# Performance work log

Measured on AMD Instinct MI355X. Metric: run time of the kernel, lower is better.

Reference implementation:

```python
import jax, jax.numpy as jnp
import numpy as np

B, LQ, LA = 128, 128, 512
VOCAB, EMB, FILT, K = 50000, 300, 400, 3
EPS = 1e-8


def setup_inputs() -> dict:
    key = jax.random.key(0)
    kq, ka, ke, kw, kb, kW = jax.random.split(key, 6)
    questions = jax.random.randint(kq, (B, LQ), 0, VOCAB + 1, dtype=jnp.int32)
    answers = jax.random.randint(ka, (B, LA), 0, VOCAB + 1, dtype=jnp.int32)
    emb = jax.random.normal(ke, (VOCAB + 1, EMB), dtype=jnp.float32) * 0.1
    emb = emb.at[0].set(0.0)  # padding_idx=0
    fan_in = EMB * K
    bound = 1.0 / np.sqrt(fan_in)
    conv_w = jax.random.uniform(kw, (FILT, EMB, K), jnp.float32, -bound, bound)
    conv_b = jax.random.uniform(kb, (FILT,), jnp.float32, -bound, bound)
    W = jax.random.normal(kW, (FILT, FILT), dtype=jnp.float32)  # init.normal_(std=1)
    return {"questions": questions, "answers": answers, "emb": emb,
            "conv_w": conv_w, "conv_b": conv_b, "W": W}


def _encode(tokens, emb, conv_w, conv_b):
    # tokens [B,L] -> embed [B,L,E] -> transpose to NCH [B,E,L] -> conv1d pad=1
    x = emb[tokens].transpose(0, 2, 1)
    y = jax.lax.conv_general_dilated(
        x, conv_w, window_strides=(1,), padding=[(1, 1)],
        dimension_numbers=("NCH", "OIH", "NCH"))
    return y + conv_b[None, :, None]  # [B, FILT, L]


def reference(questions, answers, emb, conv_w, conv_b, W):
    Q = _encode(questions, emb, conv_w, conv_b)  # [B,F,Lq]
    A = _encode(answers, emb, conv_w, conv_b)    # [B,F,La]
    # G = tanh(Q^T W A)  -> [B, Lq, La]
    G = jnp.tanh(jnp.einsum("bfq,fg,bga->bqa", Q, W, A))
    roQ = jax.nn.softmax(jnp.max(G, axis=2), axis=1)  # [B,Lq]
    roA = jax.nn.softmax(jnp.max(G, axis=1), axis=1)  # [B,La]
    rQ = jnp.einsum("bfq,bq->bf", Q, roQ)  # [B,F]
    rA = jnp.einsum("bfa,ba->bf", A, roA)  # [B,F]
    nQ = jnp.maximum(jnp.linalg.norm(rQ, axis=1), EPS)
    nA = jnp.maximum(jnp.linalg.norm(rA, axis=1), EPS)
    return jnp.sum(rQ * rA, axis=1) / (nQ * nA)  # [B]
```

## Files before the change

kernel.cpp:

```cpp
#include <hip/hip_runtime.h>
#include <hip/hip_bf16.h>

#define BB   128
#define LQ   128
#define LA   512
#define EMBD 300
#define FILT 400
#define KW   3

#define NT   25
#define KC   30
#define KCF  13
#define MT   64

typedef unsigned short u16;
typedef unsigned int   u32;
typedef __attribute__((ext_vector_type(4))) int    i32x4;
typedef __attribute__((ext_vector_type(4))) float  f32x4;
typedef __attribute__((ext_vector_type(8))) __bf16 bf16x8;

__device__ __forceinline__ u16 f2b(float f){
  u32 u = __float_as_uint(f);
  u32 r = (u + 0x7FFFu + ((u >> 16) & 1u)) >> 16;
  return (u16)r;
}
__device__ __forceinline__ u32 encf(float f){
  u32 u = __float_as_uint(f);
  return (u & 0x80000000u) ? ~u : (u | 0x80000000u);
}
__device__ __forceinline__ float decf(u32 k){
  u32 u = (k & 0x80000000u) ? (k ^ 0x80000000u) : ~k;
  return __uint_as_float(u);
}
__device__ __forceinline__ bf16x8 bzero(){
  i32x4 z; z.x = 0; z.y = 0; z.z = 0; z.w = 0;
  return __builtin_bit_cast(bf16x8, z);
}

__global__ void k_prep(const float* __restrict__ cw, const float* __restrict__ W,
                       u32* __restrict__ wTf, u32* __restrict__ wF){
  int idx = blockIdx.x * 256 + threadIdx.x;
  const int N1 = KC * NT * 64;
  const int N2 = KCF * NT * 64;
  if (idx < N1){
    int kc  = idx / (NT * 64);
    int rem = idx - kc * (NT * 64);
    int nt  = rem >> 6;
    int lane = rem & 63;
    int n = nt * 16 + (lane & 15);
    int quad = lane >> 4;
    u32 pack[4];
    #pragma unroll
    for (int d = 0; d < 4; d++){
      u16 h[2];
      #pragma unroll
      for (int s = 0; s < 2; s++){
        int kp = kc * 32 + quad * 8 + 2 * d + s;
        int kk = kp / 320, e = kp - kk * 320;
        float v = (e < EMBD) ? cw[(size_t)n * (EMBD * KW) + e * KW + kk] : 0.f;
        h[s] = f2b(v);
      }
      pack[d] = (u32)h[0] | ((u32)h[1] << 16);
    }
    i32x4 o; o.x = pack[0]; o.y = pack[1]; o.z = pack[2]; o.w = pack[3];
    *((i32x4*)wTf + idx) = o;
  } else if (idx < N1 + N2){
    int id2 = idx - N1;
    int kc  = id2 / (NT * 64);
    int rem = id2 - kc * (NT * 64);
    int nt  = rem >> 6;
    int lane = rem & 63;
    int n = nt * 16 + (lane & 15);
    int quad = lane >> 4;
    u32 pack[4];
    #pragma unroll
    for (int d = 0; d < 4; d++){
      u16 h[2];
      #pragma unroll
      for (int s = 0; s < 2; s++){
        int k = kc * 32 + quad * 8 + 2 * d + s;
        float v = (k < FILT) ? W[(size_t)k * FILT + n] : 0.f;
        h[s] = f2b(v);
      }
      pack[d] = (u32)h[0] | ((u32)h[1] << 16);
    }
    i32x4 o; o.x = pack[0]; o.y = pack[1]; o.z = pack[2]; o.w = pack[3];
    *((i32x4*)wF + id2) = o;
  }
}

__global__ __launch_bounds__(512, 4) void k_encode_all(const int* __restrict__ qtok,
    const int* __restrict__ atok, const float* __restrict__ emb,
    const u32* __restrict__ wTf, const float* __restrict__ bias,
    u16* __restrict__ outQ, u16* __restrict__ outA){
  __shared__ u16 At[66 * 328];

  const int tid  = threadIdx.x;
  const int w    = tid >> 6;
  const int lane = tid & 63;
  const int col  = lane & 15;
  const int quad = lane >> 4;
  const bool has4 = (w == 0);
  const int nA = BB * LA / MT;
  const bool isA = ((int)blockIdx.x < nA);
  const int bi = isA ? blockIdx.x : (blockIdx.x - nA);
  const int L  = isA ? LA : LQ;
  const int* toks = isA ? atok : qtok;
  u16* out = isA ? outA : outQ;
  const int row0 = bi * MT;
  const int b    = row0 / L;
  const int l0   = row0 - b * L;

  int tk[10], cc[10], rws[10];
  #pragma unroll
  for (int u = 0; u < 10; u++){
    int idx = tid + 512 * u;
    tk[u] = -1; cc[u] = 0; rws[u] = 0;
    if (idx < 66 * 75){
      int r = idx / 75, c4 = idx - r * 75;
      int pos = l0 - 1 + r;
      cc[u] = c4;
      rws[u] = (r * 328 + c4 * 4) >> 1;
      if ((unsigned)pos < (unsigned)L) tk[u] = toks[b * L + pos];
    }
  }
  for (int i = tid; i < 66 * 328 / 2; i += 512) ((u32*)At)[i] = 0u;
  __syncthreads();
  {
    const float4* emb4 = (const float4*)emb;
    #pragma unroll
    for (int g = 0; g < 2; g++){
      float4 v[5];
      #pragma unroll
      for (int u = 0; u < 5; u++){
        int uu = g * 5 + u;
        if (tk[uu] >= 0) v[u] = emb4[(size_t)tk[uu] * 75 + cc[uu]];
      }
      #pragma unroll
      for (int u = 0; u < 5; u++){
        int uu = g * 5 + u;
        if (tk[uu] >= 0){
          u32 p0 = (u32)f2b(v[u].x) | ((u32)f2b(v[u].y) << 16);
          u32 p1 = (u32)f2b(v[u].z) | ((u32)f2b(v[u].w) << 16);
          ((u32*)At)[rws[uu]]     = p0;
          ((u32*)At)[rws[uu] + 1] = p1;
        }
      }
    }
  }

  f32x4 acc[4][4];
  #pragma unroll
  for (int j = 0; j < 4; j++)
    #pragma unroll
    for (int mf = 0; mf < 4; mf++)
      acc[j][mf] = (f32x4){0.f, 0.f, 0.f, 0.f};

  __syncthreads();

  const i32x4* wTfp = (const i32x4*)wTf;
  i32x4 Bb[2][4];
  {
    #pragma unroll
    for (int j = 0; j < 3; j++) Bb[0][j] = wTfp[(size_t)(w + 8 * j) * 64 + lane];
    if (has4) Bb[0][3] = wTfp[(size_t)24 * 64 + lane];
  }
  #pragma unroll
  for (int kc = 0; kc < KC; kc++){
    const int cur = kc & 1;
    if (kc + 1 < KC){
      const i32x4* s = wTfp + (size_t)(kc + 1) * (NT * 64) + lane;
      #pragma unroll
      for (int j = 0; j < 3; j++) Bb[cur ^ 1][j] = s[(w + 8 * j) * 64];
      if (has4) Bb[cur ^ 1][3] = s[24 * 64];
    }
    const int kk = kc / 10, e0 = (kc - kk * 10) * 32;
    const int ebase = e0 + quad * 8;
    bf16x8 a[4];
    #pragma unroll
    for (int mf = 0; mf < 4; mf++)
      a[mf] = __builtin_bit_cast(bf16x8, *(const i32x4*)(At + (mf * 16 + col + kk) * 328 + ebase));
    #pragma unroll
    for (int j = 0; j < 3; j++){
      bf16x8 bf = __builtin_bit_cast(bf16x8, Bb[cur][j]);
      #pragma unroll
      for (int mf = 0; mf < 4; mf++)
        acc[j][mf] = __builtin_amdgcn_mfma_f32_16x16x32_bf16(a[mf], bf, acc[j][mf], 0, 0, 0);
    }
    if (has4){
      bf16x8 bf = __builtin_bit_cast(bf16x8, Bb[cur][3]);
      #pragma unroll
      for (int mf = 0; mf < 4; mf++)
        acc[3][mf] = __builtin_amdgcn_mfma_f32_16x16x32_bf16(a[mf], bf, acc[3][mf], 0, 0, 0);
    }
  }

  #pragma unroll
  for (int j = 0; j < 4; j++){
    if (j == 3 && !has4) continue;
    int n = ((j < 3) ? (w + 8 * j) : 24) * 16 + col;
    float bv = bias[n];
    #pragma unroll
    for (int mf = 0; mf < 4; mf++){
      int rbase = row0 + mf * 16 + quad * 4;
      #pragma unroll
      for (int r = 0; r < 4; r++)
        out[(size_t)(rbase + r) * FILT + n] = f2b(acc[j][mf][r] + bv);
    }
  }
}

__global__ __launch_bounds__(512) void k_mid(const u16* __restrict__ QT,
    const u32* __restrict__ wF, const u16* __restrict__ AT,
    u32* __restrict__ rme, u32* __restrict__ cme){
  __shared__ u16 Ts[64 * 408];
  __shared__ float cpart[512][5];
  const int tid  = threadIdx.x;
  const int w    = tid >> 6;
  const int lane = tid & 63;
  const int col  = lane & 15;
  const int quad = lane >> 4;
  const int qh   = blockIdx.x;
  const int b    = blockIdx.y;
  const int wq   = w & 3;
  const int wh   = w >> 2;

  {
    const int bnt = wh ? 13 : 0;
    const int cnt = wh ? 12 : 13;
    const u16* arow = QT + (size_t)(b * LQ + qh * 64 + wq * 16 + col) * FILT;
    const i32x4* wFp = (const i32x4*)wF;
    for (int ntc = 0; ntc < 3; ntc++){
      const int nleft = cnt - ntc * 5;
      f32x4 acc[5];
      #pragma unroll
      for (int j = 0; j < 5; j++) acc[j] = (f32x4){0.f, 0.f, 0.f, 0.f};
      i32x4 Ab[2], Bb[2][5];
      Ab[0] = *(const i32x4*)(arow + quad * 8);
      #pragma unroll
      for (int j = 0; j < 5; j++)
        if (j < nleft) Bb[0][j] = wFp[(size_t)(bnt + ntc * 5 + j) * 64 + lane];
      for (int kc = 0; kc < KCF; kc++){
        const int cur = kc & 1;
        if (kc + 1 < KCF){
          Ab[cur ^ 1] = *(const i32x4*)(arow + (kc + 1) * 32 + quad * 8);
          #pragma unroll
          for (int j = 0; j < 5; j++)
            if (j < nleft)
              Bb[cur ^ 1][j] = wFp[((size_t)(kc + 1) * NT + bnt + ntc * 5 + j) * 64 + lane];
        }
        bf16x8 a = __builtin_bit_cast(bf16x8, Ab[cur]);
        #pragma unroll
        for (int j = 0; j < 5; j++)
          if (j < nleft)
            acc[j] = __builtin_amdgcn_mfma_f32_16x16x32_bf16(a,
                       __builtin_bit_cast(bf16x8, Bb[cur][j]), acc[j], 0, 0, 0);
      }
      #pragma unroll
      for (int j = 0; j < 5; j++){
        if (j < nleft){
          int g = (bnt + ntc * 5 + j) * 16 + col;
          #pragma unroll
          for (int r = 0; r < 4; r++)
            Ts[(wq * 16 + quad * 4 + r) * 408 + g] = f2b(acc[j][r]);
        }
      }
    }
  }
  __syncthreads();

  float rm[4];
  #pragma unroll
  for (int r = 0; r < 4; r++) rm[r] = -3.4e38f;
  const u16* Tsrow = Ts + (wq * 16 + col) * 408;
  for (int atg = 0; atg < 2; atg++){
    f32x4 acc[8];
    #pragma unroll
    for (int i = 0; i < 8; i++) acc[i] = (f32x4){0.f, 0.f, 0.f, 0.f};
    const u16* ar = AT + (size_t)(b * LA + wh * 256 + atg * 128 + col) * FILT;
    i32x4 Ab2[2], Bb2[2][8];
    Ab2[0] = *(const i32x4*)(Tsrow + quad * 8);
    #pragma unroll
    for (int i = 0; i < 8; i++)
      Bb2[0][i] = *(const i32x4*)(ar + (size_t)(i * 16) * FILT + quad * 8);
    for (int kc = 0; kc < KCF; kc++){
      const int cur = kc & 1;
      if (kc + 1 < KCF){
        int off = (kc + 1) * 32 + quad * 8;
        Ab2[cur ^ 1] = *(const i32x4*)(Tsrow + off);
        #pragma unroll
        for (int i = 0; i < 8; i++)
          Bb2[cur ^ 1][i] = *(const i32x4*)(ar + (size_t)(i * 16) * FILT + off);
      }
      const bool live = (kc < 12) || (quad < 2);
      bf16x8 a = live ? __builtin_bit_cast(bf16x8, Ab2[cur]) : bzero();
      #pragma unroll
      for (int i = 0; i < 8; i++)
        acc[i] = __builtin_amdgcn_mfma_f32_16x16x32_bf16(a,
                   __builtin_bit_cast(bf16x8, Bb2[cur][i]), acc[i], 0, 0, 0);
    }
    #pragma unroll
    for (int i = 0; i < 8; i++){
      float cmx = fmaxf(fmaxf(acc[i][0], acc[i][1]), fmaxf(acc[i][2], acc[i][3]));
      cmx = fmaxf(cmx, __shfl_xor(cmx, 16));
      cmx = fmaxf(cmx, __shfl_xor(cmx, 32));
      if (quad == 0) cpart[wh * 256 + atg * 128 + i * 16 + col][wq] = cmx;
      #pragma unroll
      for (int r = 0; r < 4; r++) rm[r] = fmaxf(rm[r], acc[i][r]);
    }
  }
  #pragma unroll
  for (int r = 0; r < 4; r++){
    float m = rm[r];
    m = fmaxf(m, __shfl_xor(m, 1));
    m = fmaxf(m, __shfl_xor(m, 2));
    m = fmaxf(m, __shfl_xor(m, 4));
    m = fmaxf(m, __shfl_xor(m, 8));
    if (col == 0)
      atomicMax(&rme[b * LQ + qh * 64 + wq * 16 + quad * 4 + r], encf(m));
  }
  __syncthreads();
  {
    float m = cpart[tid][0];
    #pragma unroll
    for (int s = 1; s < 4; s++) m = fmaxf(m, cpart[tid][s]);
    atomicMax(&cme[b * LA + tid], encf(m));
  }
}

__global__ __launch_bounds__(256) void k_pool(const u16* __restrict__ QT,
    const u16* __restrict__ AT, const u32* __restrict__ rme,
    const u32* __restrict__ cme, float* __restrict__ rqp, float* __restrict__ rap){
  __shared__ float sq[128];
  __shared__ float sa[512];
  __shared__ float red[4];
  const int s = blockIdx.x, b = blockIdx.y, tid = threadIdx.x;
  if (tid < 128) sq[tid] = tanhf(decf(rme[b * LQ + tid]));
  sa[tid]       = tanhf(decf(cme[b * LA + tid]));
  sa[tid + 256] = tanhf(decf(cme[b * LA + 256 + tid]));
  __syncthreads();
  if (tid < 64){
    float m = fmaxf(sq[tid], sq[tid + 64]);
    #pragma unroll
    for (int off = 32; off; off >>= 1) m = fmaxf(m, __shfl_down(m, off));
    if (tid == 0) red[0] = m;
  } else if (tid < 128){
    int l = tid - 64;
    float m = sa[l];
    #pragma unroll
    for (int i = 1; i < 8; i++) m = fmaxf(m, sa[l + 64 * i]);
    #pragma unroll
    for (int off = 32; off; off >>= 1) m = fmaxf(m, __shfl_down(m, off));
    if (l == 0) red[1] = m;
  }
  __syncthreads();
  if (tid < 128) sq[tid] = __expf(sq[tid] - red[0]);
  sa[tid]       = __expf(sa[tid] - red[1]);
  sa[tid + 256] = __expf(sa[tid + 256] - red[1]);
  __syncthreads();
  if (tid < 64){
    float v = sq[tid] + sq[tid + 64];
    #pragma unroll
    for (int off = 32; off; off >>= 1) v += __shfl_down(v, off);
    if (tid == 0) red[2] = v;
  } else if (tid < 128){
    int l = tid - 64;
    float v = 0.f;
    #pragma unroll
    for (int i = 0; i < 8; i++) v += sa[l + 64 * i];
    #pragma unroll
    for (int off = 32; off; off >>= 1) v += __shfl_down(v, off);
    if (l == 0) red[3] = v;
  }
  __syncthreads();
  if (tid < 128) sq[tid] *= (1.f / red[2]);
  sa[tid]       *= (1.f / red[3]);
  sa[tid + 256] *= (1.f / red[3]);
  __syncthreads();
  if (tid < FILT / 2){
    const u32* qp = (const u32*)(QT + (size_t)(b * LQ + s * 32) * FILT) + tid;
    const u32* ap = (const u32*)(AT + (size_t)(b * LA + s * 128) * FILT) + tid;
    float rq0 = 0.f, rq1 = 0.f, ra0 = 0.f, ra1 = 0.f;
    for (int q = 0; q < 32; q++){
      u32 u = qp[q * (FILT / 2)];
      float wv = sq[s * 32 + q];
      rq0 += __uint_as_float(u << 16) * wv;
      rq1 += __uint_as_float(u & 0xFFFF0000u) * wv;
    }
    for (int a = 0; a < 128; a++){
      u32 u = ap[a * (FILT / 2)];
      float wv = sa[s * 128 + a];
      ra0 += __uint_as_float(u << 16) * wv;
      ra1 += __uint_as_float(u & 0xFFFF0000u) * wv;
    }
    size_t base = ((size_t)b * 4 + s) * FILT + 2 * tid;
    rqp[base] = rq0; rqp[base + 1] = rq1;
    rap[base] = ra0; rap[base + 1] = ra1;
  }
}

__global__ __launch_bounds__(256) void k_cos(const float* __restrict__ rqp,
    const float* __restrict__ rap, float* __restrict__ outp){
  __shared__ float rd[4], r1[4], r2[4];
  int b = blockIdx.x, tid = threadIdx.x;
  int lane = tid & 63, w = tid >> 6;
  float d = 0.f, n1 = 0.f, n2 = 0.f;
  for (int f = tid; f < FILT; f += 256){
    size_t base = (size_t)b * 4 * FILT + f;
    float rq = rqp[base] + rqp[base + FILT] + rqp[base + 2 * FILT] + rqp[base + 3 * FILT];
    float ra = rap[base] + rap[base + FILT] + rap[base + 2 * FILT] + rap[base + 3 * FILT];
    d += rq * ra; n1 += rq * rq; n2 += ra * ra;
  }
  #pragma unroll
  for (int off = 32; off; off >>= 1){
    d  += __shfl_down(d, off);
    n1 += __shfl_down(n1, off);
    n2 += __shfl_down(n2, off);
  }
  if (lane == 0){ rd[w] = d; r1[w] = n1; r2[w] = n2; }
  __syncthreads();
  if (tid == 0){
    float D  = rd[0] + rd[1] + rd[2] + rd[3];
    float N1 = r1[0] + r1[1] + r1[2] + r1[3];
    float N2 = r2[0] + r2[1] + r2[2] + r2[3];
    outp[b] = D / (fmaxf(sqrtf(N1), 1e-8f) * fmaxf(sqrtf(N2), 1e-8f));
  }
}

extern "C" void kernel_launch(void* const* d_in, const int* in_sizes, int n_in,
                              void* d_out, int out_size, void* d_ws, size_t ws_size,
                              hipStream_t stream){
  const int*   qtok = (const int*)d_in[0];
  const int*   atok = (const int*)d_in[1];
  const float* emb  = (const float*)d_in[2];
  const float* cw   = (const float*)d_in[3];
  const float* cb   = (const float*)d_in[4];
  const float* W    = (const float*)d_in[5];
  float* outp = (float*)d_out;

  char* ws = (char*)d_ws;
  size_t off = 0;
  auto alloc = [&](size_t bytes) -> char* {
    char* p = ws + off;
    off = (off + bytes + 255) & ~(size_t)255;
    return p;
  };
  u32*   wTf = (u32*)alloc((size_t)KC * NT * 64 * 16);
  u32*   wF  = (u32*)alloc((size_t)KCF * NT * 64 * 16);
  u16*   QT  = (u16*)alloc((size_t)BB * LQ * FILT * 2);
  u16*   AT  = (u16*)alloc((size_t)BB * LA * FILT * 2);
  u32*   rme = (u32*)alloc((size_t)BB * LQ * 4);
  u32*   cme = (u32*)alloc((size_t)BB * LA * 4);
  float* rqp = (float*)alloc((size_t)BB * 4 * FILT * 4);
  float* rap = (float*)alloc((size_t)BB * 4 * FILT * 4);

  hipMemsetAsync(rme, 0, (size_t)BB * LQ * 4 + (size_t)BB * LA * 4, stream);

  const int NPREP = KC * NT * 64 + KCF * NT * 64;
  const int nA = BB * LA / MT;
  const int nQ = BB * LQ / MT;
  k_prep<<<dim3((NPREP + 255) / 256), 256, 0, stream>>>(cw, W, wTf, wF);
  k_encode_all<<<dim3(nA + nQ), 512, 0, stream>>>(qtok, atok, emb, wTf, cb, QT, AT);
  k_mid<<<dim3(2, BB), 512, 0, stream>>>(QT, wF, AT, rme, cme);
  k_pool<<<dim3(4, BB), 256, 0, stream>>>(QT, AT, rme, cme, rqp, rap);
  k_cos<<<dim3(BB), 256, 0, stream>>>(rqp, rap, outp);
}
```

Measured before the change: 234.6 us.

## Split k_mid into 32-row query tiles, widen pool split, fold memset into prep

k_mid now handles 32 query rows per block instead of 64, doubling the grid to 4x128 blocks. The first GEMM is reorganised so each wave owns a set of N tiles across both 16-row fragments, and the second GEMM uses half the A tiles per wave. LDS use drops and launch bounds now request two blocks per CU. k_pool is split into 8 slices with the partial buffers and k_cos widened to match, and the rme/cme zeroing moves from hipMemsetAsync into k_prep. The intent is more parallelism and occupancy and one fewer launch, at the cost of reloading the W fragments per block and more atomics.

```diff
diff --git a/kernel.cpp b/kernel.cpp
--- a/kernel.cpp
+++ b/kernel.cpp
@@ -38,10 +38,12 @@
 }
 
 __global__ void k_prep(const float* __restrict__ cw, const float* __restrict__ W,
-                       u32* __restrict__ wTf, u32* __restrict__ wF){
+                       u32* __restrict__ wTf, u32* __restrict__ wF,
+                       u32* __restrict__ rmecme){
   int idx = blockIdx.x * 256 + threadIdx.x;
   const int N1 = KC * NT * 64;
   const int N2 = KCF * NT * 64;
+  const int N3 = BB * (LQ + LA);
   if (idx < N1){
     int kc  = idx / (NT * 64);
     int rem = idx - kc * (NT * 64);
@@ -86,6 +88,8 @@
     }
     i32x4 o; o.x = pack[0]; o.y = pack[1]; o.z = pack[2]; o.w = pack[3];
     *((i32x4*)wF + id2) = o;
+  } else if (idx < N1 + N2 + N3){
+    rmecme[idx - N1 - N2] = 0u;
   }
 }
 
@@ -210,78 +214,91 @@
   }
 }
 
-__global__ __launch_bounds__(512) void k_mid(const u16* __restrict__ QT,
+__global__ __launch_bounds__(512, 2) void k_mid(const u16* __restrict__ QT,
     const u32* __restrict__ wF, const u16* __restrict__ AT,
     u32* __restrict__ rme, u32* __restrict__ cme){
-  __shared__ u16 Ts[64 * 408];
-  __shared__ float cpart[512][5];
+  __shared__ u16 Ts[32 * 408];
+  __shared__ float cpart[512][3];
   const int tid  = threadIdx.x;
   const int w    = tid >> 6;
   const int lane = tid & 63;
   const int col  = lane & 15;
   const int quad = lane >> 4;
-  const int qh   = blockIdx.x;
+  const int qq   = blockIdx.x;
   const int b    = blockIdx.y;
-  const int wq   = w & 3;
-  const int wh   = w >> 2;
 
   {
-    const int bnt = wh ? 13 : 0;
-    const int cnt = wh ? 12 : 13;
-    const u16* arow = QT + (size_t)(b * LQ + qh * 64 + wq * 16 + col) * FILT;
+    const bool has4 = (w == 0);
+    const u16* arow0 = QT + (size_t)(b * LQ + qq * 32 + col) * FILT;
+    const u16* arow1 = QT + (size_t)(b * LQ + qq * 32 + 16 + col) * FILT;
     const i32x4* wFp = (const i32x4*)wF;
-    for (int ntc = 0; ntc < 3; ntc++){
-      const int nleft = cnt - ntc * 5;
-      f32x4 acc[5];
-      #pragma unroll
-      for (int j = 0; j < 5; j++) acc[j] = (f32x4){0.f, 0.f, 0.f, 0.f};
-      i32x4 Ab[2], Bb[2][5];
-      Ab[0] = *(const i32x4*)(arow + quad * 8);
-      #pragma unroll
-      for (int j = 0; j < 5; j++)
-        if (j < nleft) Bb[0][j] = wFp[(size_t)(bnt + ntc * 5 + j) * 64 + lane];
-      for (int kc = 0; kc < KCF; kc++){
-        const int cur = kc & 1;
-        if (kc + 1 < KCF){
-          Ab[cur ^ 1] = *(const i32x4*)(arow + (kc + 1) * 32 + quad * 8);
-          #pragma unroll
-          for (int j = 0; j < 5; j++)
-            if (j < nleft)
-              Bb[cur ^ 1][j] = wFp[((size_t)(kc + 1) * NT + bnt + ntc * 5 + j) * 64 + lane];
-        }
-        bf16x8 a = __builtin_bit_cast(bf16x8, Ab[cur]);
+    f32x4 acc1[4][2];
+    #pragma unroll
+    for (int j = 0; j < 4; j++)
+      #pragma unroll
+      for (int mf = 0; mf < 2; mf++)
+        acc1[j][mf] = (f32x4){0.f, 0.f, 0.f, 0.f};
+    i32x4 Ab[2][2], Bb[2][4];
+    {
+      Ab[0][0] = *(const i32x4*)(arow0 + quad * 8);
+      Ab[0][1] = *(const i32x4*)(arow1 + quad * 8);
+      #pragma unroll
+      for (int j = 0; j < 3; j++) Bb[0][j] = wFp[(size_t)(w + 8 * j) * 64 + lane];
+      if (has4) Bb[0][3] = wFp[(size_t)24 * 64 + lane];
+    }
+    for (int kc = 0; kc < KCF; kc++){
+      const int cur = kc & 1;
+      if (kc + 1 < KCF){
+        int off = (kc + 1) * 32 + quad * 8;
+        Ab[cur ^ 1][0] = *(const i32x4*)(arow0 + off);
+        Ab[cur ^ 1][1] = *(const i32x4*)(arow1 + off);
+        const i32x4* s = wFp + (size_t)(kc + 1) * (NT * 64) + lane;
         #pragma unroll
-        for (int j = 0; j < 5; j++)
-          if (j < nleft)
-            acc[j] = __builtin_amdgcn_mfma_f32_16x16x32_bf16(a,
-                       __builtin_bit_cast(bf16x8, Bb[cur][j]), acc[j], 0, 0, 0);
-      }
-      #pragma unroll
-      for (int j = 0; j < 5; j++){
-        if (j < nleft){
-          int g = (bnt + ntc * 5 + j) * 16 + col;
-          #pragma unroll
-          for (int r = 0; r < 4; r++)
-            Ts[(wq * 16 + quad * 4 + r) * 408 + g] = f2b(acc[j][r]);
-        }
-      }
-    }
-  }
-  __syncthreads();
-
+        for (int j = 0; j < 3; j++) Bb[cur ^ 1][j] = s[(w + 8 * j) * 64];
+        if (has4) Bb[cur ^ 1][3] = s[24 * 64];
+      }
+      bf16x8 a0 = __builtin_bit_cast(bf16x8, Ab[cur][0]);
+      bf16x8 a1 = __builtin_bit_cast(bf16x8, Ab[cur][1]);
+      #pragma unroll
+      for (int j = 0; j < 3; j++){
+        bf16x8 bf = __builtin_bit_cast(bf16x8, Bb[cur][j]);
+        acc1[j][0] = __builtin_amdgcn_mfma_f32_16x16x32_bf16(a0, bf, acc1[j][0], 0, 0, 0);
+        acc1[j][1] = __builtin_amdgcn_mfma_f32_16x16x32_bf16(a1, bf, acc1[j][1], 0, 0, 0);
+      }
+      if (has4){
+        bf16x8 bf = __builtin_bit_cast(bf16x8, Bb[cur][3]);
+        acc1[3][0] = __builtin_amdgcn_mfma_f32_16x16x32_bf16(a0, bf, acc1[3][0], 0, 0, 0);
+        acc1[3][1] = __builtin_amdgcn_mfma_f32_16x16x32_bf16(a1, bf, acc1[3][1], 0, 0, 0);
+      }
+    }
+    #pragma unroll
+    for (int j = 0; j < 4; j++){
+      if (j == 3 && !has4) continue;
+      int g = ((j < 3) ? (w + 8 * j) : 24) * 16 + col;
+      #pragma unroll
+      for (int mf = 0; mf < 2; mf++)
+        #pragma unroll
+        for (int r = 0; r < 4; r++)
+          Ts[(mf * 16 + quad * 4 + r) * 408 + g] = f2b(acc1[j][mf][r]);
+    }
+  }
+  __syncthreads();
+
+  const int qt2 = w & 1;
+  const int aq  = w >> 1;
   float rm[4];
   #pragma unroll
   for (int r = 0; r < 4; r++) rm[r] = -3.4e38f;
-  const u16* Tsrow = Ts + (wq * 16 + col) * 408;
+  const u16* Tsrow = Ts + (qt2 * 16 + col) * 408;
   for (int atg = 0; atg < 2; atg++){
-    f32x4 acc[8];
-    #pragma unroll
-    for (int i = 0; i < 8; i++) acc[i] = (f32x4){0.f, 0.f, 0.f, 0.f};
-    const u16* ar = AT + (size_t)(b * LA + wh * 256 + atg * 128 + col) * FILT;
-    i32x4 Ab2[2], Bb2[2][8];
+    f32x4 acc[4];
+    #pragma unroll
+    for (int i = 0; i < 4; i++) acc[i] = (f32x4){0.f, 0.f, 0.f, 0.f};
+    const u16* ar = AT + (size_t)(b * LA + aq * 128 + atg * 64 + col) * FILT;
+    i32x4 Ab2[2], Bb2[2][4];
     Ab2[0] = *(const i32x4*)(Tsrow + quad * 8);
     #pragma unroll
-    for (int i = 0; i < 8; i++)
+    for (int i = 0; i < 4; i++)
       Bb2[0][i] = *(const i32x4*)(ar + (size_t)(i * 16) * FILT + quad * 8);
     for (int kc = 0; kc < KCF; kc++){
       const int cur = kc & 1;
@@ -289,22 +306,22 @@
         int off = (kc + 1) * 32 + quad * 8;
         Ab2[cur ^ 1] = *(const i32x4*)(Tsrow + off);
         #pragma unroll
-        for (int i = 0; i < 8; i++)
+        for (int i = 0; i < 4; i++)
           Bb2[cur ^ 1][i] = *(const i32x4*)(ar + (size_t)(i * 16) * FILT + off);
       }
       const bool live = (kc < 12) || (quad < 2);
       bf16x8 a = live ? __builtin_bit_cast(bf16x8, Ab2[cur]) : bzero();
       #pragma unroll
-      for (int i = 0; i < 8; i++)
+      for (int i = 0; i < 4; i++)
         acc[i] = __builtin_amdgcn_mfma_f32_16x16x32_bf16(a,
                    __builtin_bit_cast(bf16x8, Bb2[cur][i]), acc[i], 0, 0, 0);
     }
     #pragma unroll
-    for (int i = 0; i < 8; i++){
+    for (int i = 0; i < 4; i++){
       float cmx = fmaxf(fmaxf(acc[i][0], acc[i][1]), fmaxf(acc[i][2], acc[i][3]));
       cmx = fmaxf(cmx, __shfl_xor(cmx, 16));
       cmx = fmaxf(cmx, __shfl_xor(cmx, 32));
-      if (quad == 0) cpart[wh * 256 + atg * 128 + i * 16 + col][wq] = cmx;
+      if (quad == 0) cpart[aq * 128 + atg * 64 + i * 16 + col][qt2] = cmx;
       #pragma unroll
       for (int r = 0; r < 4; r++) rm[r] = fmaxf(rm[r], acc[i][r]);
     }
@@ -317,13 +334,11 @@
     m = fmaxf(m, __shfl_xor(m, 4));
     m = fmaxf(m, __shfl_xor(m, 8));
     if (col == 0)
-      atomicMax(&rme[b * LQ + qh * 64 + wq * 16 + quad * 4 + r], encf(m));
+      atomicMax(&rme[b * LQ + qq * 32 + qt2 * 16 + quad * 4 + r], encf(m));
   }
   __syncthreads();
   {
-    float m = cpart[tid][0];
-    #pragma unroll
-    for (int s = 1; s < 4; s++) m = fmaxf(m, cpart[tid][s]);
+    float m = fmaxf(cpart[tid][0], cpart[tid][1]);
     atomicMax(&cme[b * LA + tid], encf(m));
   }
 }
@@ -378,22 +393,22 @@
   sa[tid + 256] *= (1.f / red[3]);
   __syncthreads();
   if (tid < FILT / 2){
-    const u32* qp = (const u32*)(QT + (size_t)(b * LQ + s * 32) * FILT) + tid;
-    const u32* ap = (const u32*)(AT + (size_t)(b * LA + s * 128) * FILT) + tid;
+    const u32* qp = (const u32*)(QT + (size_t)(b * LQ + s * 16) * FILT) + tid;
+    const u32* ap = (const u32*)(AT + (size_t)(b * LA + s * 64) * FILT) + tid;
     float rq0 = 0.f, rq1 = 0.f, ra0 = 0.f, ra1 = 0.f;
-    for (int q = 0; q < 32; q++){
+    for (int q = 0; q < 16; q++){
       u32 u = qp[q * (FILT / 2)];
-      float wv = sq[s * 32 + q];
+      float wv = sq[s * 16 + q];
       rq0 += __uint_as_float(u << 16) * wv;
       rq1 += __uint_as_float(u & 0xFFFF0000u) * wv;
     }
-    for (int a = 0; a < 128; a++){
+    for (int a = 0; a < 64; a++){
       u32 u = ap[a * (FILT / 2)];
-      float wv = sa[s * 128 + a];
+      float wv = sa[s * 64 + a];
       ra0 += __uint_as_float(u << 16) * wv;
       ra1 += __uint_as_float(u & 0xFFFF0000u) * wv;
     }
-    size_t base = ((size_t)b * 4 + s) * FILT + 2 * tid;
+    size_t base = ((size_t)b * 8 + s) * FILT + 2 * tid;
     rqp[base] = rq0; rqp[base + 1] = rq1;
     rap[base] = ra0; rap[base + 1] = ra1;
   }
@@ -406,9 +421,13 @@
   int lane = tid & 63, w = tid >> 6;
   float d = 0.f, n1 = 0.f, n2 = 0.f;
   for (int f = tid; f < FILT; f += 256){
-    size_t base = (size_t)b * 4 * FILT + f;
-    float rq = rqp[base] + rqp[base + FILT] + rqp[base + 2 * FILT] + rqp[base + 3 * FILT];
-    float ra = rap[base] + rap[base + FILT] + rap[base + 2 * FILT] + rap[base + 3 * FILT];
+    size_t base = (size_t)b * 8 * FILT + f;
+    float rq = 0.f, ra = 0.f;
+    #pragma unroll
+    for (int s = 0; s < 8; s++){
+      rq += rqp[base + s * FILT];
+      ra += rap[base + s * FILT];
+    }
     d += rq * ra; n1 += rq * rq; n2 += ra * ra;
   }
   #pragma unroll
@@ -451,17 +470,15 @@
   u16*   AT  = (u16*)alloc((size_t)BB * LA * FILT * 2);
   u32*   rme = (u32*)alloc((size_t)BB * LQ * 4);
   u32*   cme = (u32*)alloc((size_t)BB * LA * 4);
-  float* rqp = (float*)alloc((size_t)BB * 4 * FILT * 4);
-  float* rap = (float*)alloc((size_t)BB * 4 * FILT * 4);
-
-  hipMemsetAsync(rme, 0, (size_t)BB * LQ * 4 + (size_t)BB * LA * 4, stream);
-
-  const int NPREP = KC * NT * 64 + KCF * NT * 64;
+  float* rqp = (float*)alloc((size_t)BB * 8 * FILT * 4);
+  float* rap = (float*)alloc((size_t)BB * 8 * FILT * 4);
+
+  const int NPREP = KC * NT * 64 + KCF * NT * 64 + BB * (LQ + LA);
   const int nA = BB * LA / MT;
   const int nQ = BB * LQ / MT;
-  k_prep<<<dim3((NPREP + 255) / 256), 256, 0, stream>>>(cw, W, wTf, wF);
+  k_prep<<<dim3((NPREP + 255) / 256), 256, 0, stream>>>(cw, W, wTf, wF, rme);
   k_encode_all<<<dim3(nA + nQ), 512, 0, stream>>>(qtok, atok, emb, wTf, cb, QT, AT);
-  k_mid<<<dim3(2, BB), 512, 0, stream>>>(QT, wF, AT, rme, cme);
-  k_pool<<<dim3(4, BB), 256, 0, stream>>>(QT, AT, rme, cme, rqp, rap);
+  k_mid<<<dim3(4, BB), 512, 0, stream>>>(QT, wF, AT, rme, cme);
+  k_pool<<<dim3(8, BB), 256, 0, stream>>>(QT, AT, rme, cme, rqp, rap);
   k_cos<<<dim3(BB), 256, 0, stream>>>(rqp, rap, outp);
 }
```

New measurement: 237.3 us. No clear change (+1.1%).
